# Optimization experiments

Measured on AMD Instinct MI355X. Metric: run time of the kernel, lower is better.

The kernel has to match this reference:

```python
import jax, jax.numpy as jnp
import numpy as np

HIDDEN = 1024
HEADS = 16
HEAD_DIM = HIDDEN // HEADS
B, S = 2, 2048


def setup_inputs() -> dict:
    key = jax.random.key(0)
    ks = jax.random.split(key, 7)
    scale = 1.0 / np.sqrt(HIDDEN)
    return {
        "hidden_states": jax.random.normal(ks[0], (B, S, HIDDEN), dtype=jnp.float32),
        "Wq": jax.random.normal(ks[1], (HIDDEN, HIDDEN), dtype=jnp.float32) * scale,
        "bq": jax.random.normal(ks[2], (HIDDEN,), dtype=jnp.float32) * 0.02,
        "Wk": jax.random.normal(ks[3], (HIDDEN, HIDDEN), dtype=jnp.float32) * scale,
        "bk": jax.random.normal(ks[4], (HIDDEN,), dtype=jnp.float32) * 0.02,
        "Wv": jax.random.normal(ks[5], (HIDDEN, HIDDEN), dtype=jnp.float32) * scale,
        "bv": jax.random.normal(ks[6], (HIDDEN,), dtype=jnp.float32) * 0.02,
    }


def reference(hidden_states, Wq, bq, Wk, bk, Wv, bv):
    # QKV projections: [B,S,H] -> [B,S,heads,head_dim]
    def proj(W, b):
        y = jnp.einsum('bsh,hd->bsd', hidden_states, W) + b
        return y.reshape(B, S, HEADS, HEAD_DIM)

    q = proj(Wq, bq)
    k = proj(Wk, bk)
    v = proj(Wv, bv)

    # scores: [B,heads,Sq,Sk]
    scores = jnp.einsum('bqnd,bknd->bnqk', q, k) / jnp.sqrt(
        jnp.asarray(HEAD_DIM, dtype=hidden_states.dtype))
    probs = jax.nn.softmax(scores, axis=-1)  # dropout is identity at inference
    ctx = jnp.einsum('bnqk,bknd->bqnd', probs, v)
    return ctx.reshape(B, S, HIDDEN)
```

## Files before the change

kernel.cpp:

```cpp
#include <hip/hip_runtime.h>

#define HID 1024
#define SEQ 2048
#define NB  2
#define NH  16
#define HD  64
#define M_ROWS (NB*SEQ)

typedef _Float16 half8 __attribute__((ext_vector_type(8)));
typedef _Float16 half4 __attribute__((ext_vector_type(4)));
typedef float    f32x4 __attribute__((ext_vector_type(4)));
typedef unsigned uint4v __attribute__((ext_vector_type(4)));

#define GLOAD_LDS16(g, l) \
  __builtin_amdgcn_global_load_lds((const __attribute__((address_space(1))) void*)(g), \
                                   (__attribute__((address_space(3))) void*)(l), 16, 0, 0)

#define QSCL 0.18033688011112042f

#define CVT_PK_U32(a, b) __builtin_bit_cast(unsigned, __builtin_amdgcn_cvt_pkrtz((a), (b)))

__device__ __forceinline__ float exp2_raw(float x) {
  float r;
  asm("v_exp_f32 %0, %1" : "=v"(r) : "v"(x));
  return r;
}


__global__ __launch_bounds__(256) void cvt_x(const float* __restrict__ in,
                                             _Float16* __restrict__ out, int n4) {
  int i = blockIdx.x * 256 + threadIdx.x;
  int stride = gridDim.x * 256;
  for (; i < n4; i += stride) {
    float4 v = ((const float4*)in)[i];
    half4 o;
    o[0] = (_Float16)v.x; o[1] = (_Float16)v.y;
    o[2] = (_Float16)v.z; o[3] = (_Float16)v.w;
    ((half4*)out)[i] = o;
  }
}

__global__ __launch_bounds__(256) void cvt_w(const float* __restrict__ W0,
                                             const float* __restrict__ W1,
                                             const float* __restrict__ W2,
                                             _Float16* __restrict__ Wt) {
  __shared__ __align__(16) _Float16 tl[64 * 72];
  const int z = blockIdx.z;
  const float* W = (z == 0) ? W0 : (z == 1) ? W1 : W2;
  const int k0 = blockIdx.x * 64, n0 = blockIdx.y * 64;
  const int tid = threadIdx.x;
  const int kk = tid >> 4;
  const int nn = (tid & 15) * 4;
#pragma unroll
  for (int r = 0; r < 4; ++r) {
    int k = kk + r * 16;
    float4 v = *(const float4*)&W[(size_t)(k0 + k) * HID + n0 + nn];
    tl[(nn + 0) * 72 + k] = (_Float16)v.x;
    tl[(nn + 1) * 72 + k] = (_Float16)v.y;
    tl[(nn + 2) * 72 + k] = (_Float16)v.z;
    tl[(nn + 3) * 72 + k] = (_Float16)v.w;
  }
  __syncthreads();
#pragma unroll
  for (int r = 0; r < 2; ++r) {
    int c = r * 256 + tid;
    int n = c >> 3, kc = (c & 7) * 8;
    half8 o = *(const half8*)&tl[n * 72 + kc];
    *(half8*)&Wt[(size_t)z * HID * HID + (size_t)(n0 + n) * HID + k0 + kc] = o;
  }
}

__global__ __launch_bounds__(512, 6) void qkv_gemm(const _Float16* __restrict__ X,
                                                   const _Float16* __restrict__ Wt,
                                                   const float* __restrict__ bq,
                                                   const float* __restrict__ bk,
                                                   const float* __restrict__ bv,
                                                   _Float16* __restrict__ QKV,
                                                   _Float16* __restrict__ Vt) {
  __shared__ __align__(16) _Float16 Al[128 * 64];
  __shared__ __align__(16) _Float16 Bl[128 * 64];
  const int tid = threadIdx.x;
  const int lane = tid & 63;
  const int wid = tid >> 6;
  const int wr = wid >> 2;
  const int wc = wid & 3;
  const int g = lane >> 4, qi = lane & 15;
  const int r0 = blockIdx.x * 128;
  const int c0 = blockIdx.y * 128;
  const int z = blockIdx.z;
  const _Float16* Wz = Wt + (size_t)z * HID * HID;
  const float* bias = (z == 0) ? bq : (z == 1) ? bk : bv;
  const float scl = (z == 0) ? QSCL : 1.0f;
  _Float16* Out = QKV + (size_t)z * M_ROWS * HID;

  f32x4 acc[4][2];
#pragma unroll
  for (int m = 0; m < 4; ++m)
#pragma unroll
    for (int n = 0; n < 2; ++n) acc[m][n] = (f32x4){0.f, 0.f, 0.f, 0.f};

  int offA[2][4], offB[2][2];
#pragma unroll
  for (int ks = 0; ks < 2; ++ks) {
#pragma unroll
    for (int m = 0; m < 4; ++m) {
      int row = wr * 64 + m * 16 + qi;
      offA[ks][m] = row * 64 + (((ks * 4 + g) ^ (row & 7)) * 8);
    }
#pragma unroll
    for (int n = 0; n < 2; ++n) {
      int col = wc * 32 + n * 16 + qi;
      offB[ks][n] = col * 64 + (((ks * 4 + g) ^ (col & 7)) * 8);
    }
  }

  for (int kt = 0; kt < 16; ++kt) {
    const int kb = kt * 64;
#pragma unroll
    for (int it = 0; it < 2; ++it) {
      int c = it * 512 + tid;
      int row = c >> 3, ci = c & 7;
      int sc = (ci ^ (row & 7)) * 8;
      GLOAD_LDS16(X + (size_t)(r0 + row) * HID + kb + sc, &Al[c * 8]);
      GLOAD_LDS16(Wz + (size_t)(c0 + row) * HID + kb + sc, &Bl[c * 8]);
    }
    __syncthreads();
#pragma unroll
    for (int ks = 0; ks < 2; ++ks) {
      half8 a[4], b[2];
#pragma unroll
      for (int m = 0; m < 4; ++m) a[m] = *(const half8*)&Al[offA[ks][m]];
#pragma unroll
      for (int n = 0; n < 2; ++n) b[n] = *(const half8*)&Bl[offB[ks][n]];
#pragma unroll
      for (int m = 0; m < 4; ++m)
#pragma unroll
        for (int n = 0; n < 2; ++n)
          acc[m][n] = __builtin_amdgcn_mfma_f32_16x16x32_f16(a[m], b[n], acc[m][n], 0, 0, 0);
    }
    __syncthreads();
  }

  if (z == 2) {
    const int b = r0 >> 11;
    const int r0s = r0 & (SEQ - 1);
#pragma unroll
    for (int n = 0; n < 2; ++n) {
      int col = c0 + wc * 32 + n * 16 + qi;
      float bv_ = bv[col];
      int h = col >> 6, d = col & 63;
      _Float16* vrow = Vt + ((size_t)(b * NH + h) * HD + d) * SEQ;
#pragma unroll
      for (int m = 0; m < 4; ++m) {
        int sp = r0s + wr * 64 + 32 * (m >> 1) + 8 * g + 4 * (m & 1);
        half4 hv;
#pragma unroll
        for (int r = 0; r < 4; ++r) hv[r] = (_Float16)(acc[m][n][r] + bv_);
        *(half4*)&vrow[sp] = hv;
      }
    }
  } else {
#pragma unroll
    for (int n = 0; n < 2; ++n) {
      int col = c0 + wc * 32 + n * 16 + qi;
      float bv_ = bias[col];
#pragma unroll
      for (int m = 0; m < 4; ++m) {
        int row = r0 + wr * 64 + m * 16 + g * 4;
#pragma unroll
        for (int r = 0; r < 4; ++r)
          Out[(size_t)(row + r) * HID + col] = (_Float16)((acc[m][n][r] + bv_) * scl);
      }
    }
  }
}

__global__ __launch_bounds__(512, 4) void attn(const _Float16* __restrict__ Q,
                                               const _Float16* __restrict__ K,
                                               const _Float16* __restrict__ Vt,
                                               float* __restrict__ Out) {
  __shared__ __align__(16) _Float16 Kl[4][64 * 64];
  __shared__ __align__(16) _Float16 Vl[4][64 * 64];

  const int tid = threadIdx.x;
  const int lane = tid & 63;
  const int w = tid >> 6;
  const int g = lane >> 4, qi = lane & 15;
  const int nl = (blockIdx.x & 7) * 32 + (blockIdx.x >> 3);
  const int qb = nl & 7;
  const int bh = nl >> 3;
  const int b = bh >> 4, h = bh & 15;
  const size_t baseq = (size_t)b * SEQ * HID + (size_t)h * HD;
  const size_t basev = (size_t)bh * HD * SEQ;
  const int q0 = qb * 256 + w * 32;

  half8 qf[2][2];
#pragma unroll
  for (int cfr = 0; cfr < 2; ++cfr)
#pragma unroll
    for (int ks = 0; ks < 2; ++ks)
      qf[cfr][ks] = *(const half8*)&Q[baseq + (size_t)(q0 + cfr * 16 + qi) * HID + ks * 32 + g * 8];

  half8 ones;
#pragma unroll
  for (int j = 0; j < 8; ++j) ones[j] = (qi == 0) ? (_Float16)1.0f : (_Float16)0.0f;

  int offA[2][4];
#pragma unroll
  for (int ks = 0; ks < 2; ++ks)
#pragma unroll
    for (int fr = 0; fr < 4; ++fr) {
      int row = fr * 16 + qi;
      offA[ks][fr] = row * 64 + (((ks * 4 + g) ^ (row & 7)) * 8);
    }

  f32x4 ctx[4][2];
#pragma unroll
  for (int fr = 0; fr < 4; ++fr)
#pragma unroll
    for (int cfr = 0; cfr < 2; ++cfr) ctx[fr][cfr] = (f32x4){0.f, 0.f, 0.f, 0.f};
  f32x4 c5[2] = {(f32x4){0.f, 0.f, 0.f, 0.f}, (f32x4){0.f, 0.f, 0.f, 0.f}};

#define STAGE(buf, tt) do {                                                        \
    const int kv_ = (tt) * 64;                                                     \
    int row_ = tid >> 3, ci_ = tid & 7;                                            \
    int sc_ = (ci_ ^ (row_ & 7)) * 8;                                              \
    GLOAD_LDS16(K + baseq + (size_t)(kv_ + row_) * HID + sc_, &Kl[buf][tid * 8]);  \
    GLOAD_LDS16(Vt + basev + (size_t)row_ * SEQ + kv_ + sc_, &Vl[buf][tid * 8]);   \
  } while (0)

  STAGE(0, 0);
  STAGE(1, 1);

  for (int t = 0; t < 32; ++t) {
    const int cur = t & 3;
    const int nt = (t + 2 < 32) ? t + 2 : 31;
    STAGE((t + 2) & 3, nt);
    asm volatile("s_waitcnt vmcnt(4)" ::: "memory");
    __builtin_amdgcn_s_barrier();
    asm volatile("" ::: "memory");

    f32x4 sf[4][2];
#pragma unroll
    for (int fr = 0; fr < 4; ++fr)
#pragma unroll
      for (int cfr = 0; cfr < 2; ++cfr) sf[fr][cfr] = (f32x4){0.f, 0.f, 0.f, 0.f};
    __builtin_amdgcn_s_setprio(1);
#pragma unroll
    for (int ks = 0; ks < 2; ++ks) {
      half8 ak[4];
#pragma unroll
      for (int fr = 0; fr < 4; ++fr) ak[fr] = *(const half8*)&Kl[cur][offA[ks][fr]];
#pragma unroll
      for (int fr = 0; fr < 4; ++fr)
#pragma unroll
        for (int cfr = 0; cfr < 2; ++cfr)
          sf[fr][cfr] = __builtin_amdgcn_mfma_f32_16x16x32_f16(ak[fr], qf[cfr][ks], sf[fr][cfr], 0, 0, 0);
    }
    __builtin_amdgcn_s_setprio(0);

    unsigned wp[2][8];
#pragma unroll
    for (int cfr = 0; cfr < 2; ++cfr)
#pragma unroll
      for (int fr = 0; fr < 4; ++fr) {
        wp[cfr][2 * fr]     = CVT_PK_U32(exp2_raw(sf[fr][cfr][0]), exp2_raw(sf[fr][cfr][1]));
        wp[cfr][2 * fr + 1] = CVT_PK_U32(exp2_raw(sf[fr][cfr][2]), exp2_raw(sf[fr][cfr][3]));
      }

    __builtin_amdgcn_s_setprio(1);
#pragma unroll
    for (int ks = 0; ks < 2; ++ks) {
      half8 av[4];
#pragma unroll
      for (int fr = 0; fr < 4; ++fr) av[fr] = *(const half8*)&Vl[cur][offA[ks][fr]];
      half8 pb[2];
#pragma unroll
      for (int cfr = 0; cfr < 2; ++cfr) {
        uint4v uu = {wp[cfr][4 * ks], wp[cfr][4 * ks + 1], wp[cfr][4 * ks + 2], wp[cfr][4 * ks + 3]};
        pb[cfr] = __builtin_bit_cast(half8, uu);
      }
#pragma unroll
      for (int fr = 0; fr < 4; ++fr)
#pragma unroll
        for (int cfr = 0; cfr < 2; ++cfr)
          ctx[fr][cfr] = __builtin_amdgcn_mfma_f32_16x16x32_f16(av[fr], pb[cfr], ctx[fr][cfr], 0, 0, 0);
#pragma unroll
      for (int cfr = 0; cfr < 2; ++cfr)
        c5[cfr] = __builtin_amdgcn_mfma_f32_16x16x32_f16(ones, pb[cfr], c5[cfr], 0, 0, 0);
    }
    __builtin_amdgcn_s_setprio(0);
  }
#undef STAGE
  asm volatile("s_waitcnt vmcnt(0)" ::: "memory");

#pragma unroll
  for (int cfr = 0; cfr < 2; ++cfr) {
    float tot = __shfl(c5[cfr][0], qi, 64);
    float inv = 1.f / tot;
    int qrow = q0 + cfr * 16 + qi;
#pragma unroll
    for (int fr = 0; fr < 4; ++fr) {
      float4 o;
      o.x = ctx[fr][cfr][0] * inv;
      o.y = ctx[fr][cfr][1] * inv;
      o.z = ctx[fr][cfr][2] * inv;
      o.w = ctx[fr][cfr][3] * inv;
      *(float4*)&Out[baseq + (size_t)qrow * HID + fr * 16 + g * 4] = o;
    }
  }
}


extern "C" void kernel_launch(void* const* d_in, const int* in_sizes, int n_in,
                              void* d_out, int out_size, void* d_ws, size_t ws_size,
                              hipStream_t stream) {
  (void)in_sizes; (void)n_in; (void)out_size; (void)ws_size;
  const float* hs = (const float*)d_in[0];
  const float* Wq = (const float*)d_in[1];
  const float* bq = (const float*)d_in[2];
  const float* Wk = (const float*)d_in[3];
  const float* bk = (const float*)d_in[4];
  const float* Wv = (const float*)d_in[5];
  const float* bv = (const float*)d_in[6];
  float* out = (float*)d_out;

  _Float16* Xh  = (_Float16*)d_ws;
  _Float16* Wt  = Xh + (size_t)M_ROWS * HID;
  _Float16* QKV = Wt + (size_t)3 * HID * HID;
  _Float16* Vt  = QKV + (size_t)3 * M_ROWS * HID;

  cvt_x<<<1024, 256, 0, stream>>>(hs, Xh, (M_ROWS * HID) / 4);
  cvt_w<<<dim3(16, 16, 3), 256, 0, stream>>>(Wq, Wk, Wv, Wt);
  qkv_gemm<<<dim3(32, 8, 3), 512, 0, stream>>>(Xh, Wt, bq, bk, bv, QKV, Vt);
  attn<<<256, 512, 0, stream>>>(QKV,
                                QKV + (size_t)M_ROWS * HID,
                                Vt,
                                out);
}
```

Baseline: 85.40 us.

## Software-pipeline attention loop so PV of previous tile overlaps current exp

Restructures the attention main loop so the P·V MFMAs for tile t-1 are issued after the QK MFMAs of tile t and before the exp/convert of tile t. This lets the transcendental work overlap the matrix-core work, with a final PV step after the loop. The barrier and wait now come before staging the next tile, and launch bounds drop to 2 blocks per CU so the extra live P registers fit. Lower occupancy is the main risk, and the 4-buffer ring must still cover the one-tile lag on the V buffer.

```diff
diff --git a/kernel.cpp b/kernel.cpp
--- a/kernel.cpp
+++ b/kernel.cpp
@@ -175,7 +175,7 @@
   }
 }
 
-__global__ __launch_bounds__(512, 4) void attn(const _Float16* __restrict__ Q,
+__global__ __launch_bounds__(512, 2) void attn(const _Float16* __restrict__ Q,
                                                const _Float16* __restrict__ K,
                                                const _Float16* __restrict__ Vt,
                                                float* __restrict__ Out) {
@@ -220,6 +220,7 @@
 #pragma unroll
     for (int cfr = 0; cfr < 2; ++cfr) ctx[fr][cfr] = (f32x4){0.f, 0.f, 0.f, 0.f};
   f32x4 c5[2] = {(f32x4){0.f, 0.f, 0.f, 0.f}, (f32x4){0.f, 0.f, 0.f, 0.f}};
+  unsigned wp[2][8];
 
 #define STAGE(buf, tt) do {                                                        \
     const int kv_ = (tt) * 64;                                                     \
@@ -229,16 +230,44 @@
     GLOAD_LDS16(Vt + basev + (size_t)row_ * SEQ + kv_ + sc_, &Vl[buf][tid * 8]);   \
   } while (0)
 
+#define PV_STEP(tt) do {                                                            \
+    const int pv_ = (tt) & 3;                                                       \
+    __builtin_amdgcn_s_setprio(1);                                                  \
+    _Pragma("unroll")                                                               \
+    for (int ks = 0; ks < 2; ++ks) {                                                \
+      half8 av[4];                                                                  \
+      _Pragma("unroll")                                                             \
+      for (int fr = 0; fr < 4; ++fr) av[fr] = *(const half8*)&Vl[pv_][offA[ks][fr]];\
+      half8 pb[2];                                                                  \
+      _Pragma("unroll")                                                             \
+      for (int cfr = 0; cfr < 2; ++cfr) {                                           \
+        uint4v uu = {wp[cfr][4 * ks], wp[cfr][4 * ks + 1],                          \
+                     wp[cfr][4 * ks + 2], wp[cfr][4 * ks + 3]};                     \
+        pb[cfr] = __builtin_bit_cast(half8, uu);                                    \
+      }                                                                             \
+      _Pragma("unroll")                                                             \
+      for (int fr = 0; fr < 4; ++fr)                                                \
+        _Pragma("unroll")                                                           \
+        for (int cfr = 0; cfr < 2; ++cfr)                                           \
+          ctx[fr][cfr] = __builtin_amdgcn_mfma_f32_16x16x32_f16(av[fr], pb[cfr],    \
+                                                                ctx[fr][cfr], 0, 0, 0); \
+      _Pragma("unroll")                                                             \
+      for (int cfr = 0; cfr < 2; ++cfr)                                             \
+        c5[cfr] = __builtin_amdgcn_mfma_f32_16x16x32_f16(ones, pb[cfr], c5[cfr], 0, 0, 0); \
+    }                                                                               \
+    __builtin_amdgcn_s_setprio(0);                                                  \
+  } while (0)
+
   STAGE(0, 0);
   STAGE(1, 1);
 
   for (int t = 0; t < 32; ++t) {
     const int cur = t & 3;
+    asm volatile("s_waitcnt vmcnt(2)" ::: "memory");
+    __builtin_amdgcn_s_barrier();
+    asm volatile("" ::: "memory");
     const int nt = (t + 2 < 32) ? t + 2 : 31;
     STAGE((t + 2) & 3, nt);
-    asm volatile("s_waitcnt vmcnt(4)" ::: "memory");
-    __builtin_amdgcn_s_barrier();
-    asm volatile("" ::: "memory");
 
     f32x4 sf[4][2];
 #pragma unroll
@@ -259,7 +288,8 @@
     }
     __builtin_amdgcn_s_setprio(0);
 
-    unsigned wp[2][8];
+    if (t > 0) PV_STEP(t - 1);
+
 #pragma unroll
     for (int cfr = 0; cfr < 2; ++cfr)
 #pragma unroll
@@ -267,32 +297,12 @@
         wp[cfr][2 * fr]     = CVT_PK_U32(exp2_raw(sf[fr][cfr][0]), exp2_raw(sf[fr][cfr][1]));
         wp[cfr][2 * fr + 1] = CVT_PK_U32(exp2_raw(sf[fr][cfr][2]), exp2_raw(sf[fr][cfr][3]));
       }
-
-    __builtin_amdgcn_s_setprio(1);
-#pragma unroll
-    for (int ks = 0; ks < 2; ++ks) {
-      half8 av[4];
-#pragma unroll
-      for (int fr = 0; fr < 4; ++fr) av[fr] = *(const half8*)&Vl[cur][offA[ks][fr]];
-      half8 pb[2];
-#pragma unroll
-      for (int cfr = 0; cfr < 2; ++cfr) {
-        uint4v uu = {wp[cfr][4 * ks], wp[cfr][4 * ks + 1], wp[cfr][4 * ks + 2], wp[cfr][4 * ks + 3]};
-        pb[cfr] = __builtin_bit_cast(half8, uu);
-      }
-#pragma unroll
-      for (int fr = 0; fr < 4; ++fr)
-#pragma unroll
-        for (int cfr = 0; cfr < 2; ++cfr)
-          ctx[fr][cfr] = __builtin_amdgcn_mfma_f32_16x16x32_f16(av[fr], pb[cfr], ctx[fr][cfr], 0, 0, 0);
-#pragma unroll
-      for (int cfr = 0; cfr < 2; ++cfr)
-        c5[cfr] = __builtin_amdgcn_mfma_f32_16x16x32_f16(ones, pb[cfr], c5[cfr], 0, 0, 0);
-    }
-    __builtin_amdgcn_s_setprio(0);
-  }
+  }
+
+  asm volatile("s_waitcnt vmcnt(0)" ::: "memory");
+  PV_STEP(31);
+#undef PV_STEP
 #undef STAGE
-  asm volatile("s_waitcnt vmcnt(0)" ::: "memory");
 
 #pragma unroll
   for (int cfr = 0; cfr < 2; ++cfr) {
```

New measurement: 92.16 us. +7.9%, slower.

## Split attention KV range across two blocks and add a combine kernel

Applied to the files above, without the earlier changes.

Splits each attention block's key/value sequence into two halves handled by separate blocks, doubling the grid from 256 to 512 blocks to fill more compute units. Each half writes unnormalized partial context (fp32 for one half into the output buffer, fp16 for the other into reused workspace) plus per-row softmax denominators. A new combine kernel sums the partials and normalizes. This relies on the kernel already lacking a running max, so partials add directly. It costs an extra kernel launch and extra global memory traffic, and the fp16 partial loses some precision.

```diff
diff --git a/kernel.cpp b/kernel.cpp
--- a/kernel.cpp
+++ b/kernel.cpp
@@ -178,7 +178,9 @@
 __global__ __launch_bounds__(512, 4) void attn(const _Float16* __restrict__ Q,
                                                const _Float16* __restrict__ K,
                                                const _Float16* __restrict__ Vt,
-                                               float* __restrict__ Out) {
+                                               float* __restrict__ P0,
+                                               _Float16* __restrict__ P1,
+                                               float* __restrict__ Sums) {
   __shared__ __align__(16) _Float16 Kl[4][64 * 64];
   __shared__ __align__(16) _Float16 Vl[4][64 * 64];
 
@@ -186,13 +188,15 @@
   const int lane = tid & 63;
   const int w = tid >> 6;
   const int g = lane >> 4, qi = lane & 15;
-  const int nl = (blockIdx.x & 7) * 32 + (blockIdx.x >> 3);
-  const int qb = nl & 7;
-  const int bh = nl >> 3;
+  const int nl = (blockIdx.x & 7) * 64 + (blockIdx.x >> 3);
+  const int half = nl & 1;
+  const int qb = (nl >> 1) & 7;
+  const int bh = nl >> 4;
   const int b = bh >> 4, h = bh & 15;
   const size_t baseq = (size_t)b * SEQ * HID + (size_t)h * HD;
   const size_t basev = (size_t)bh * HD * SEQ;
   const int q0 = qb * 256 + w * 32;
+  const int kw = half * 16;
 
   half8 qf[2][2];
 #pragma unroll
@@ -229,12 +233,12 @@
     GLOAD_LDS16(Vt + basev + (size_t)row_ * SEQ + kv_ + sc_, &Vl[buf][tid * 8]);   \
   } while (0)
 
-  STAGE(0, 0);
-  STAGE(1, 1);
-
-  for (int t = 0; t < 32; ++t) {
+  STAGE(0, kw);
+  STAGE(1, kw + 1);
+
+  for (int t = 0; t < 16; ++t) {
     const int cur = t & 3;
-    const int nt = (t + 2 < 32) ? t + 2 : 31;
+    const int nt = (t + 2 < 16) ? kw + t + 2 : kw + 15;
     STAGE((t + 2) & 3, nt);
     asm volatile("s_waitcnt vmcnt(4)" ::: "memory");
     __builtin_amdgcn_s_barrier();
@@ -294,20 +298,51 @@
 #undef STAGE
   asm volatile("s_waitcnt vmcnt(0)" ::: "memory");
 
+  float* sums = Sums + half * (32 * SEQ) + bh * SEQ;
 #pragma unroll
   for (int cfr = 0; cfr < 2; ++cfr) {
-    float tot = __shfl(c5[cfr][0], qi, 64);
-    float inv = 1.f / tot;
     int qrow = q0 + cfr * 16 + qi;
-#pragma unroll
-    for (int fr = 0; fr < 4; ++fr) {
-      float4 o;
-      o.x = ctx[fr][cfr][0] * inv;
-      o.y = ctx[fr][cfr][1] * inv;
-      o.z = ctx[fr][cfr][2] * inv;
-      o.w = ctx[fr][cfr][3] * inv;
-      *(float4*)&Out[baseq + (size_t)qrow * HID + fr * 16 + g * 4] = o;
-    }
+    if (g == 0) sums[qrow] = c5[cfr][0];
+    if (half == 0) {
+#pragma unroll
+      for (int fr = 0; fr < 4; ++fr) {
+        float4 o;
+        o.x = ctx[fr][cfr][0]; o.y = ctx[fr][cfr][1];
+        o.z = ctx[fr][cfr][2]; o.w = ctx[fr][cfr][3];
+        *(float4*)&P0[baseq + (size_t)qrow * HID + fr * 16 + g * 4] = o;
+      }
+    } else {
+#pragma unroll
+      for (int fr = 0; fr < 4; ++fr) {
+        half4 hv;
+#pragma unroll
+        for (int r = 0; r < 4; ++r) hv[r] = (_Float16)ctx[fr][cfr][r];
+        *(half4*)&P1[baseq + (size_t)qrow * HID + fr * 16 + g * 4] = hv;
+      }
+    }
+  }
+}
+
+__global__ __launch_bounds__(256) void combine(float* __restrict__ out,
+                                               const _Float16* __restrict__ p1,
+                                               const float* __restrict__ sums) {
+  int i = blockIdx.x * 256 + threadIdx.x;
+  const int nq = M_ROWS * HID / 4;
+  for (; i < nq; i += gridDim.x * 256) {
+    int e = i * 4;
+    int row = e >> 10;
+    int col = e & 1023;
+    int bh = (row >> 11) * 16 + (col >> 6);
+    int srow = row & (SEQ - 1);
+    float s = sums[bh * SEQ + srow] + sums[32 * SEQ + bh * SEQ + srow];
+    float inv = 1.0f / s;
+    float4 o = *(float4*)&out[e];
+    half4 p = *(const half4*)&p1[e];
+    o.x = (o.x + (float)p[0]) * inv;
+    o.y = (o.y + (float)p[1]) * inv;
+    o.z = (o.z + (float)p[2]) * inv;
+    o.w = (o.w + (float)p[3]) * inv;
+    *(float4*)&out[e] = o;
   }
 }
 
@@ -329,12 +364,15 @@
   _Float16* Wt  = Xh + (size_t)M_ROWS * HID;
   _Float16* QKV = Wt + (size_t)3 * HID * HID;
   _Float16* Vt  = QKV + (size_t)3 * M_ROWS * HID;
+  _Float16* P1  = Xh;
+  float*    Sums = (float*)Wt;
 
   cvt_x<<<1024, 256, 0, stream>>>(hs, Xh, (M_ROWS * HID) / 4);
   cvt_w<<<dim3(16, 16, 3), 256, 0, stream>>>(Wq, Wk, Wv, Wt);
   qkv_gemm<<<dim3(32, 8, 3), 512, 0, stream>>>(Xh, Wt, bq, bk, bv, QKV, Vt);
-  attn<<<256, 512, 0, stream>>>(QKV,
+  attn<<<512, 512, 0, stream>>>(QKV,
                                 QKV + (size_t)M_ROWS * HID,
                                 Vt,
-                                out);
-}
+                                out, P1, Sums);
+  combine<<<2048, 256, 0, stream>>>(out, P1, Sums);
+}
```

Result: slower. 92.48 us (+8.3%).

## Give each attention wave 64 query rows and replace ones-MFMA row sums with VALU sums

Applied to the files above, without the earlier changes.

The attention block shrinks from 8 waves to 4, and each wave now handles 64 query rows instead of 32, so every K/V fragment read from LDS feeds twice as many MFMAs. The key tile is processed in two halves to keep the score registers bounded. The row sum of exponentials is now accumulated with VALU adds and lane shuffles instead of an extra MFMA against a ones vector. Staging loads are split over two iterations per thread. The trade-off is higher register pressure, half as many waves per block for hiding latency, and more VALU work in the exp stage.

```diff
diff --git a/kernel.cpp b/kernel.cpp
--- a/kernel.cpp
+++ b/kernel.cpp
@@ -175,7 +175,7 @@
   }
 }
 
-__global__ __launch_bounds__(512, 4) void attn(const _Float16* __restrict__ Q,
+__global__ __launch_bounds__(256, 2) void attn(const _Float16* __restrict__ Q,
                                                const _Float16* __restrict__ K,
                                                const _Float16* __restrict__ Vt,
                                                float* __restrict__ Out) {
@@ -192,18 +192,14 @@
   const int b = bh >> 4, h = bh & 15;
   const size_t baseq = (size_t)b * SEQ * HID + (size_t)h * HD;
   const size_t basev = (size_t)bh * HD * SEQ;
-  const int q0 = qb * 256 + w * 32;
-
-  half8 qf[2][2];
-#pragma unroll
-  for (int cfr = 0; cfr < 2; ++cfr)
+  const int q0 = qb * 256 + w * 64;
+
+  half8 qf[4][2];
+#pragma unroll
+  for (int cfr = 0; cfr < 4; ++cfr)
 #pragma unroll
     for (int ks = 0; ks < 2; ++ks)
       qf[cfr][ks] = *(const half8*)&Q[baseq + (size_t)(q0 + cfr * 16 + qi) * HID + ks * 32 + g * 8];
-
-  half8 ones;
-#pragma unroll
-  for (int j = 0; j < 8; ++j) ones[j] = (qi == 0) ? (_Float16)1.0f : (_Float16)0.0f;
 
   int offA[2][4];
 #pragma unroll
@@ -214,19 +210,23 @@
       offA[ks][fr] = row * 64 + (((ks * 4 + g) ^ (row & 7)) * 8);
     }
 
-  f32x4 ctx[4][2];
+  f32x4 ctx[4][4];
 #pragma unroll
   for (int fr = 0; fr < 4; ++fr)
 #pragma unroll
-    for (int cfr = 0; cfr < 2; ++cfr) ctx[fr][cfr] = (f32x4){0.f, 0.f, 0.f, 0.f};
-  f32x4 c5[2] = {(f32x4){0.f, 0.f, 0.f, 0.f}, (f32x4){0.f, 0.f, 0.f, 0.f}};
-
-#define STAGE(buf, tt) do {                                                        \
-    const int kv_ = (tt) * 64;                                                     \
-    int row_ = tid >> 3, ci_ = tid & 7;                                            \
-    int sc_ = (ci_ ^ (row_ & 7)) * 8;                                              \
-    GLOAD_LDS16(K + baseq + (size_t)(kv_ + row_) * HID + sc_, &Kl[buf][tid * 8]);  \
-    GLOAD_LDS16(Vt + basev + (size_t)row_ * SEQ + kv_ + sc_, &Vl[buf][tid * 8]);   \
+    for (int cfr = 0; cfr < 4; ++cfr) ctx[fr][cfr] = (f32x4){0.f, 0.f, 0.f, 0.f};
+  float lsum[4] = {0.f, 0.f, 0.f, 0.f};
+
+#define STAGE(buf, tt) do {                                                          \
+    const int kv_ = (tt) * 64;                                                       \
+    _Pragma("unroll")                                                                \
+    for (int it_ = 0; it_ < 2; ++it_) {                                              \
+      int c_ = it_ * 256 + tid;                                                      \
+      int row_ = c_ >> 3, ci_ = c_ & 7;                                              \
+      int sc_ = (ci_ ^ (row_ & 7)) * 8;                                              \
+      GLOAD_LDS16(K + baseq + (size_t)(kv_ + row_) * HID + sc_, &Kl[buf][c_ * 8]);   \
+      GLOAD_LDS16(Vt + basev + (size_t)row_ * SEQ + kv_ + sc_, &Vl[buf][c_ * 8]);    \
+    }                                                                                \
   } while (0)
 
   STAGE(0, 0);
@@ -236,68 +236,71 @@
     const int cur = t & 3;
     const int nt = (t + 2 < 32) ? t + 2 : 31;
     STAGE((t + 2) & 3, nt);
-    asm volatile("s_waitcnt vmcnt(4)" ::: "memory");
+    asm volatile("s_waitcnt vmcnt(8)" ::: "memory");
     __builtin_amdgcn_s_barrier();
     asm volatile("" ::: "memory");
 
-    f32x4 sf[4][2];
-#pragma unroll
-    for (int fr = 0; fr < 4; ++fr)
-#pragma unroll
-      for (int cfr = 0; cfr < 2; ++cfr) sf[fr][cfr] = (f32x4){0.f, 0.f, 0.f, 0.f};
-    __builtin_amdgcn_s_setprio(1);
-#pragma unroll
-    for (int ks = 0; ks < 2; ++ks) {
-      half8 ak[4];
-#pragma unroll
-      for (int fr = 0; fr < 4; ++fr) ak[fr] = *(const half8*)&Kl[cur][offA[ks][fr]];
-#pragma unroll
-      for (int fr = 0; fr < 4; ++fr)
-#pragma unroll
-        for (int cfr = 0; cfr < 2; ++cfr)
-          sf[fr][cfr] = __builtin_amdgcn_mfma_f32_16x16x32_f16(ak[fr], qf[cfr][ks], sf[fr][cfr], 0, 0, 0);
-    }
-    __builtin_amdgcn_s_setprio(0);
-
-    unsigned wp[2][8];
-#pragma unroll
-    for (int cfr = 0; cfr < 2; ++cfr)
-#pragma unroll
-      for (int fr = 0; fr < 4; ++fr) {
-        wp[cfr][2 * fr]     = CVT_PK_U32(exp2_raw(sf[fr][cfr][0]), exp2_raw(sf[fr][cfr][1]));
-        wp[cfr][2 * fr + 1] = CVT_PK_U32(exp2_raw(sf[fr][cfr][2]), exp2_raw(sf[fr][cfr][3]));
+#pragma unroll
+    for (int kh = 0; kh < 2; ++kh) {
+      f32x4 sf[2][4];
+#pragma unroll
+      for (int fl = 0; fl < 2; ++fl)
+#pragma unroll
+        for (int cfr = 0; cfr < 4; ++cfr) sf[fl][cfr] = (f32x4){0.f, 0.f, 0.f, 0.f};
+      __builtin_amdgcn_s_setprio(1);
+#pragma unroll
+      for (int ks = 0; ks < 2; ++ks) {
+        half8 ak[2];
+#pragma unroll
+        for (int fl = 0; fl < 2; ++fl) ak[fl] = *(const half8*)&Kl[cur][offA[ks][kh * 2 + fl]];
+#pragma unroll
+        for (int fl = 0; fl < 2; ++fl)
+#pragma unroll
+          for (int cfr = 0; cfr < 4; ++cfr)
+            sf[fl][cfr] = __builtin_amdgcn_mfma_f32_16x16x32_f16(ak[fl], qf[cfr][ks], sf[fl][cfr], 0, 0, 0);
       }
-
-    __builtin_amdgcn_s_setprio(1);
-#pragma unroll
-    for (int ks = 0; ks < 2; ++ks) {
-      half8 av[4];
-#pragma unroll
-      for (int fr = 0; fr < 4; ++fr) av[fr] = *(const half8*)&Vl[cur][offA[ks][fr]];
-      half8 pb[2];
-#pragma unroll
-      for (int cfr = 0; cfr < 2; ++cfr) {
-        uint4v uu = {wp[cfr][4 * ks], wp[cfr][4 * ks + 1], wp[cfr][4 * ks + 2], wp[cfr][4 * ks + 3]};
-        pb[cfr] = __builtin_bit_cast(half8, uu);
+      __builtin_amdgcn_s_setprio(0);
+
+      unsigned wp[4][4];
+#pragma unroll
+      for (int cfr = 0; cfr < 4; ++cfr)
+#pragma unroll
+        for (int fl = 0; fl < 2; ++fl) {
+          float e0 = exp2_raw(sf[fl][cfr][0]);
+          float e1 = exp2_raw(sf[fl][cfr][1]);
+          float e2 = exp2_raw(sf[fl][cfr][2]);
+          float e3 = exp2_raw(sf[fl][cfr][3]);
+          lsum[cfr] += (e0 + e1) + (e2 + e3);
+          wp[cfr][2 * fl]     = CVT_PK_U32(e0, e1);
+          wp[cfr][2 * fl + 1] = CVT_PK_U32(e2, e3);
+        }
+
+      __builtin_amdgcn_s_setprio(1);
+      {
+        half8 av[4];
+#pragma unroll
+        for (int fr = 0; fr < 4; ++fr) av[fr] = *(const half8*)&Vl[cur][offA[kh][fr]];
+#pragma unroll
+        for (int cfr = 0; cfr < 4; ++cfr) {
+          uint4v uu = {wp[cfr][0], wp[cfr][1], wp[cfr][2], wp[cfr][3]};
+          half8 pb = __builtin_bit_cast(half8, uu);
+#pragma unroll
+          for (int fr = 0; fr < 4; ++fr)
+            ctx[fr][cfr] = __builtin_amdgcn_mfma_f32_16x16x32_f16(av[fr], pb, ctx[fr][cfr], 0, 0, 0);
+        }
       }
-#pragma unroll
-      for (int fr = 0; fr < 4; ++fr)
-#pragma unroll
-        for (int cfr = 0; cfr < 2; ++cfr)
-          ctx[fr][cfr] = __builtin_amdgcn_mfma_f32_16x16x32_f16(av[fr], pb[cfr], ctx[fr][cfr], 0, 0, 0);
-#pragma unroll
-      for (int cfr = 0; cfr < 2; ++cfr)
-        c5[cfr] = __builtin_amdgcn_mfma_f32_16x16x32_f16(ones, pb[cfr], c5[cfr], 0, 0, 0);
-    }
-    __builtin_amdgcn_s_setprio(0);
+      __builtin_amdgcn_s_setprio(0);
+    }
   }
 #undef STAGE
   asm volatile("s_waitcnt vmcnt(0)" ::: "memory");
 
 #pragma unroll
-  for (int cfr = 0; cfr < 2; ++cfr) {
-    float tot = __shfl(c5[cfr][0], qi, 64);
-    float inv = 1.f / tot;
+  for (int cfr = 0; cfr < 4; ++cfr) {
+    float s = lsum[cfr];
+    s += __shfl_xor(s, 16);
+    s += __shfl_xor(s, 32);
+    float inv = 1.f / s;
     int qrow = q0 + cfr * 16 + qi;
 #pragma unroll
     for (int fr = 0; fr < 4; ++fr) {
@@ -333,7 +336,7 @@
   cvt_x<<<1024, 256, 0, stream>>>(hs, Xh, (M_ROWS * HID) / 4);
   cvt_w<<<dim3(16, 16, 3), 256, 0, stream>>>(Wq, Wk, Wv, Wt);
   qkv_gemm<<<dim3(32, 8, 3), 512, 0, stream>>>(Xh, Wt, bq, bk, bv, QKV, Vt);
-  attn<<<256, 512, 0, stream>>>(QKV,
+  attn<<<256, 256, 0, stream>>>(QKV,
                                 QKV + (size_t)M_ROWS * HID,
                                 Vt,
                                 out);
```

After: 95.16 us. 1.11x slower.
